# Kernel tuning notes

Measured on AMD Instinct MI355X. Metric: run time of the kernel, lower is better.

The kernel has to match this reference:

```python
import jax, jax.numpy as jnp
import numpy as np

B, S, H, Q = 32, 128, 128, 3  # users, seq_len, hidden_size, quadkey_level
L = Q - 1  # number of mixing scales


def setup_inputs() -> dict:
    key = jax.random.key(0)
    ks = jax.random.split(key, 12)
    trend0 = jax.random.normal(ks[0], (B, S, H), dtype=jnp.float32)
    trend1 = jax.random.normal(ks[1], (B, S, H), dtype=jnp.float32)
    trend2 = jax.random.normal(ks[2], (B, S, H), dtype=jnp.float32)
    # Per-position prefix linears padded into dense tensors, zero-masked beyond
    # the prefix length j+1 so the ragged math is exact:
    #   W1[j, :j+1, :j+1] ~ Linear(j+1, j+1), b1[j, :j+1]
    #   W2[j, :j+1]      ~ Linear(j+1, 1),   b2[j]
    idx = jnp.arange(S)
    pm = (idx[None, :] <= idx[:, None]).astype(jnp.float32)  # [j, s]: s <= j
    W1 = jax.random.normal(ks[3], (L, S, S, S), dtype=jnp.float32) * 0.05
    W1 = W1 * pm[None, :, :, None] * pm[None, :, None, :]
    b1 = jax.random.normal(ks[4], (L, S, S), dtype=jnp.float32) * 0.05 * pm[None]
    W2 = jax.random.normal(ks[5], (L, S, S), dtype=jnp.float32) * 0.05 * pm[None]
    b2 = jax.random.normal(ks[6], (L, S), dtype=jnp.float32) * 0.05
    # shared output MLP: Linear(H,H)->GELU->Linear(H,H); stored as [in, out]
    Wm1 = jax.random.normal(ks[7], (H, H), dtype=jnp.float32) * 0.05
    bm1 = jax.random.normal(ks[8], (H,), dtype=jnp.float32) * 0.05
    Wm2 = jax.random.normal(ks[9], (H, H), dtype=jnp.float32) * 0.05
    bm2 = jax.random.normal(ks[10], (H,), dtype=jnp.float32) * 0.05
    return {"trend0": trend0, "trend1": trend1, "trend2": trend2,
            "W1": W1, "b1": b1, "W2": W2, "b2": b2,
            "Wm1": Wm1, "bm1": bm1, "Wm2": Wm2, "bm2": bm2}


def reference(trend0, trend1, trend2, W1, b1, W2, b2, Wm1, bm1, Wm2, bm2):
    gelu = lambda x: jax.nn.gelu(x, approximate=False)  # torch nn.GELU default
    mlp = lambda x: gelu(x @ Wm1 + bm1) @ Wm2 + bm2

    rev = [trend2, trend1, trend0]  # trend_list reversed
    out_low = rev[0]
    out_high = rev[1]
    outs = [out_low]
    for i in range(Q - 1):
        # vectorized ragged prefix mix: per position j, out_low[:, :j+1] (as [B,H,j+1])
        # -> Linear(j+1,j+1) -> GELU -> Linear(j+1,1). Zero-padding in W1/b1/W2
        # kills all contributions beyond the prefix (GELU(0)=0).
        y1 = jnp.einsum('bsh,jst->bhjt', out_low, W1[i]) + b1[i]  # [B,H,S,S]
        res = jnp.einsum('bhjt,jt->bjh', gelu(y1), W2[i]) + b2[i][None, :, None]
        out_high = out_high + res
        out_low = out_high
        if i + 2 <= Q - 1:
            out_high = rev[i + 2]
        out_low = mlp(out_low)
        outs.append(out_low)
    outs.reverse()
    return tuple(outs)
```

## Files before the change

### kernel.cpp

```cpp
#include <hip/hip_runtime.h>
#include <stdint.h>

#define BSH (32 * 128 * 128)

typedef __attribute__((ext_vector_type(8))) __bf16 bf16x8;
typedef __attribute__((ext_vector_type(4))) float f32x4;

__device__ __forceinline__ unsigned short f2bf(float f) {
  union { float f; unsigned u; } v; v.f = f;
  return (unsigned short)((v.u + 0x7FFFu + ((v.u >> 16) & 1u)) >> 16);
}

__device__ __forceinline__ float fast_exp2(float x) {
#if __has_builtin(__builtin_amdgcn_exp2f)
  return __builtin_amdgcn_exp2f(x);
#else
  float r; asm("v_exp_f32 %0, %1" : "=v"(r) : "v"(x)); return r;
#endif
}
__device__ __forceinline__ float fast_rcp(float x) {
#if __has_builtin(__builtin_amdgcn_rcpf)
  return __builtin_amdgcn_rcpf(x);
#else
  float r; asm("v_rcp_f32 %0, %1" : "=v"(r) : "v"(x)); return r;
#endif
}

__device__ __forceinline__ float gelu_f(float y) {
  float u = y * y;
  float p = __builtin_fmaf(u, 0.044715f, 1.0f) * y;
  float w = fast_exp2(p * 2.30220787f);
  return y - y * fast_rcp(1.0f + w);
}

__device__ __forceinline__ void transpose_block_c(const float* __restrict__ src,
                                                  unsigned short* __restrict__ dst,
                                                  unsigned short* lds) {
  const int tid = threadIdx.x;
  const float4* s4 = (const float4*)src;
#pragma unroll
  for (int it = 0; it < 16; ++it) {
    int i4 = tid + it * 256;
    float4 v = s4[i4];
    int s = i4 >> 5;
    int t0 = (i4 * 4) & 127;
    int sc = s >> 3, se = s & 7;
#pragma unroll
    for (int e = 0; e < 4; ++e) {
      int t = t0 + e;
      lds[t * 136 + ((sc ^ ((t >> 2) & 7)) << 3) + se] = f2bf(((const float*)&v)[e]);
    }
  }
  __syncthreads();
#pragma unroll
  for (int it = 0; it < 8; ++it) {
    int c = tid + it * 256;
    int tr = c >> 4, sc = c & 15;
    uint4 d = *(const uint4*)(lds + tr * 136 + ((sc ^ ((tr >> 2) & 7)) << 3));
    *(uint4*)(dst + (sc * 128 + tr) * 8) = d;
  }
}

__global__ __launch_bounds__(256) void prepass_kernel(
    const float* __restrict__ W1, const float* __restrict__ trend2,
    const float* __restrict__ Wm1, const float* __restrict__ Wm2,
    unsigned short* __restrict__ W1Tc, unsigned short* __restrict__ T2c,
    unsigned short* __restrict__ Wm1c, unsigned short* __restrict__ Wm2c,
    float* __restrict__ out2) {
  __shared__ unsigned short lds[128 * 136];
  const int bid = blockIdx.x;
  if (bid < 256) {
    int x = bid & 7, i = bid >> 3;
    int stage = i >> 4, u = i & 15;
    int m = u & 7, half = u >> 3;
    int jpp = x + 8 * m;
    int j = half ? 127 - jpp : jpp;
    int blk = stage * 128 + j;
    transpose_block_c(W1 + blk * 16384, W1Tc + blk * 16384, lds);
  } else if (bid < 288) {
    const int b = bid - 256;
    transpose_block_c(trend2 + b * 16384, T2c + b * 16384, lds);
    const float4* s4 = (const float4*)(trend2 + b * 16384);
    float4* d4 = (float4*)(out2 + b * 16384);
#pragma unroll
    for (int it = 0; it < 16; ++it)
      d4[threadIdx.x + it * 256] = s4[threadIdx.x + it * 256];
  } else if (bid == 288) {
    transpose_block_c(Wm1, Wm1c, lds);
  } else {
    transpose_block_c(Wm2, Wm2c, lds);
  }
}

__global__ __launch_bounds__(128, 3) void mix_kernel(
    const unsigned short* __restrict__ XTc,
    const unsigned short* __restrict__ W1Tj,
    const float* __restrict__ b1j,
    const float* __restrict__ W2j,
    const float* __restrict__ b2j,
    const float* __restrict__ trendR,
    unsigned short* __restrict__ xoutc) {
  const int bid = blockIdx.x;
  const int b = bid >> 6;
  const int jp = bid & 63;
  const int js = jp, jb = 127 - jp;
  const int tid = threadIdx.x;
  const int p = tid >> 6;
  const int lane = tid & 63;
  const int lane15 = lane & 15;
  const int quad = lane >> 4;

  const int nt_s = (js >> 4) + 1, ks_s = (js >> 5) + 1;
  const int nt_b = (jb >> 4) + 1, ks_b = (jb >> 5) + 1;

  const unsigned short* Bp = XTc + b * 16384 + (p * 64 + lane15) * 8;
  const unsigned short* As = W1Tj + js * 16384 + lane15 * 8;
  const unsigned short* Ab = W1Tj + jb * 16384 + lane15 * 8;
  const float C = -2.45546937f;

  bf16x8 Bv[4][4];
#pragma unroll
  for (int ks = 0; ks < 4; ++ks)
    if (ks < ks_b) {
      const int ko = (ks * 4 + quad) * 1024;
      Bv[ks][0] = *(const bf16x8*)(Bp + ko);
      Bv[ks][1] = *(const bf16x8*)(Bp + ko + 128);
      Bv[ks][2] = *(const bf16x8*)(Bp + ko + 256);
      Bv[ks][3] = *(const bf16x8*)(Bp + ko + 384);
    }

  float psum[2][4];
#pragma unroll
  for (int jj = 0; jj < 2; ++jj)
#pragma unroll
    for (int ni = 0; ni < 4; ++ni) psum[jj][ni] = 0.f;

  for (int mt = 0; mt < nt_b; ++mt) {
    f32x4 acc[4];
#pragma unroll
    for (int ni = 0; ni < 4; ++ni) { f32x4 z = {0.f, 0.f, 0.f, 0.f}; acc[ni] = z; }
    const int mo = mt * 128;
#pragma unroll
    for (int ks = 0; ks < 4; ++ks)
      if (ks < ks_b) {
        bf16x8 a = *(const bf16x8*)(Ab + (ks * 4 + quad) * 1024 + mo);
        acc[0] = __builtin_amdgcn_mfma_f32_16x16x32_bf16(a, Bv[ks][0], acc[0], 0, 0, 0);
        acc[1] = __builtin_amdgcn_mfma_f32_16x16x32_bf16(a, Bv[ks][1], acc[1], 0, 0, 0);
        acc[2] = __builtin_amdgcn_mfma_f32_16x16x32_bf16(a, Bv[ks][2], acc[2], 0, 0, 0);
        acc[3] = __builtin_amdgcn_mfma_f32_16x16x32_bf16(a, Bv[ks][3], acc[3], 0, 0, 0);
      }
    const int tb = mt * 16 + quad * 4;
    float4 b1v = *(const float4*)(b1j + jb * 128 + tb);
    float4 w2v = *(const float4*)(W2j + jb * 128 + tb);
#pragma unroll
    for (int r = 0; r < 4; ++r) {
      float b1r = ((const float*)&b1v)[r];
      float w2r = ((const float*)&w2v)[r];
      float cb = C * b1r;
      float bw = b1r * w2r;
#pragma unroll
      for (int ni = 0; ni < 4; ++ni) {
        float a = acc[ni][r];
        float m = __builtin_fmaf(a, C, cb);
        float e = fast_exp2(m);
        float rr2 = fast_rcp(1.0f + e);
        float yw = __builtin_fmaf(a, w2r, bw);
        psum[1][ni] = __builtin_fmaf(yw, rr2, psum[1][ni]);
      }
    }
  }

  for (int mt = 0; mt < nt_s; ++mt) {
    f32x4 acc[4];
#pragma unroll
    for (int ni = 0; ni < 4; ++ni) { f32x4 z = {0.f, 0.f, 0.f, 0.f}; acc[ni] = z; }
    const int mo = mt * 128;
#pragma unroll
    for (int ks = 0; ks < 2; ++ks)
      if (ks < ks_s) {
        bf16x8 a = *(const bf16x8*)(As + (ks * 4 + quad) * 1024 + mo);
        acc[0] = __builtin_amdgcn_mfma_f32_16x16x32_bf16(a, Bv[ks][0], acc[0], 0, 0, 0);
        acc[1] = __builtin_amdgcn_mfma_f32_16x16x32_bf16(a, Bv[ks][1], acc[1], 0, 0, 0);
        acc[2] = __builtin_amdgcn_mfma_f32_16x16x32_bf16(a, Bv[ks][2], acc[2], 0, 0, 0);
        acc[3] = __builtin_amdgcn_mfma_f32_16x16x32_bf16(a, Bv[ks][3], acc[3], 0, 0, 0);
      }
    const int tb = mt * 16 + quad * 4;
    float4 b1v = *(const float4*)(b1j + js * 128 + tb);
    float4 w2v = *(const float4*)(W2j + js * 128 + tb);
#pragma unroll
    for (int r = 0; r < 4; ++r) {
      float b1r = ((const float*)&b1v)[r];
      float w2r = ((const float*)&w2v)[r];
      float cb = C * b1r;
      float bw = b1r * w2r;
#pragma unroll
      for (int ni = 0; ni < 4; ++ni) {
        float a = acc[ni][r];
        float m = __builtin_fmaf(a, C, cb);
        float e = fast_exp2(m);
        float rr2 = fast_rcp(1.0f + e);
        float yw = __builtin_fmaf(a, w2r, bw);
        psum[0][ni] = __builtin_fmaf(yw, rr2, psum[0][ni]);
      }
    }
  }

#pragma unroll
  for (int jj = 0; jj < 2; ++jj)
#pragma unroll
    for (int ni = 0; ni < 4; ++ni) {
      float v = psum[jj][ni];
      v += __shfl_xor(v, 16, 64);
      v += __shfl_xor(v, 32, 64);
      psum[jj][ni] = v;
    }

  if (quad == 0) {
#pragma unroll
    for (int jj = 0; jj < 2; ++jj) {
      const int j = jj ? jb : js;
      const float bias = b2j[j];
#pragma unroll
      for (int ni = 0; ni < 4; ++ni) {
        const int h = p * 64 + ni * 16 + lane15;
        float v = psum[jj][ni] + bias + trendR[(b * 128 + j) * 128 + h];
        xoutc[b * 16384 + ((h >> 3) * 128 + j) * 8 + (h & 7)] = f2bf(v);
      }
    }
  }
}

__global__ __launch_bounds__(256) void mlp_kernel(
    const unsigned short* __restrict__ Xc,
    const unsigned short* __restrict__ Wm1c,
    const unsigned short* __restrict__ Wm2c,
    const float* __restrict__ bm1,
    const float* __restrict__ bm2,
    float* __restrict__ outf,
    unsigned short* __restrict__ outTc,
    const int write_t) {
  __shared__ __align__(16) unsigned short U[16 * 128];
  __shared__ unsigned short ldsT[16 * 136];
  const int bid = blockIdx.x;
  const int b = bid >> 3;
  const int mb = bid & 7;
  const int tid = threadIdx.x;
  const int wave = tid >> 6;
  const int lane = tid & 63;
  const int lane15 = lane & 15;
  const int quad = lane >> 4;

  const unsigned short* Xb = Xc + b * 16384;

  f32x4 acc[2];
  { f32x4 z = {0.f, 0.f, 0.f, 0.f}; acc[0] = z; acc[1] = z; }
#pragma unroll
  for (int ks = 0; ks < 4; ++ks) {
    int kq = ks * 4 + quad;
    bf16x8 a  = *(const bf16x8*)(Xb + (kq * 128 + mb * 16 + lane15) * 8);
    bf16x8 w0 = *(const bf16x8*)(Wm1c + (kq * 128 + wave * 32 + lane15) * 8);
    bf16x8 w1 = *(const bf16x8*)(Wm1c + (kq * 128 + wave * 32 + 16 + lane15) * 8);
    acc[0] = __builtin_amdgcn_mfma_f32_16x16x32_bf16(a, w0, acc[0], 0, 0, 0);
    acc[1] = __builtin_amdgcn_mfma_f32_16x16x32_bf16(a, w1, acc[1], 0, 0, 0);
  }
#pragma unroll
  for (int ni = 0; ni < 2; ++ni) {
    int n = wave * 32 + ni * 16 + lane15;
    float bv = bm1[n];
#pragma unroll
    for (int r = 0; r < 4; ++r) {
      int jr = quad * 4 + r;
      U[((n >> 3) * 16 + jr) * 8 + (n & 7)] = f2bf(gelu_f(acc[ni][r] + bv));
    }
  }
  __syncthreads();
  { f32x4 z = {0.f, 0.f, 0.f, 0.f}; acc[0] = z; acc[1] = z; }
#pragma unroll
  for (int ks = 0; ks < 4; ++ks) {
    int kq = ks * 4 + quad;
    bf16x8 a  = *(const bf16x8*)(U + (kq * 16 + lane15) * 8);
    bf16x8 w0 = *(const bf16x8*)(Wm2c + (kq * 128 + wave * 32 + lane15) * 8);
    bf16x8 w1 = *(const bf16x8*)(Wm2c + (kq * 128 + wave * 32 + 16 + lane15) * 8);
    acc[0] = __builtin_amdgcn_mfma_f32_16x16x32_bf16(a, w0, acc[0], 0, 0, 0);
    acc[1] = __builtin_amdgcn_mfma_f32_16x16x32_bf16(a, w1, acc[1], 0, 0, 0);
  }
  {
    float* outb = outf + b * 16384 + mb * 16 * 128;
#pragma unroll
    for (int ni = 0; ni < 2; ++ni) {
      int n = wave * 32 + ni * 16 + lane15;
      float bv = bm2[n];
#pragma unroll
      for (int r = 0; r < 4; ++r) {
        int jr = quad * 4 + r;
        float v = acc[ni][r] + bv;
        outb[jr * 128 + n] = v;
        if (write_t) ldsT[jr * 136 + n] = f2bf(v);
      }
    }
  }
  if (write_t) {
    __syncthreads();
    int h = tid & 127, jr8 = tid >> 7;
    unsigned short tmp[8] __attribute__((aligned(16)));
#pragma unroll
    for (int e = 0; e < 8; ++e) tmp[e] = ldsT[(jr8 * 8 + e) * 136 + h];
    *(uint4*)(outTc + b * 16384 + ((mb * 2 + jr8) * 128 + h) * 8) = *(const uint4*)tmp;
  }
}

extern "C" void kernel_launch(void* const* d_in, const int* in_sizes, int n_in,
                              void* d_out, int out_size, void* d_ws, size_t ws_size,
                              hipStream_t stream) {
  (void)in_sizes; (void)n_in; (void)out_size; (void)ws_size;
  const float* trend0 = (const float*)d_in[0];
  const float* trend1 = (const float*)d_in[1];
  const float* trend2 = (const float*)d_in[2];
  const float* W1  = (const float*)d_in[3];
  const float* b1  = (const float*)d_in[4];
  const float* W2  = (const float*)d_in[5];
  const float* b2  = (const float*)d_in[6];
  const float* Wm1 = (const float*)d_in[7];
  const float* bm1 = (const float*)d_in[8];
  const float* Wm2 = (const float*)d_in[9];
  const float* bm2 = (const float*)d_in[10];
  float* out = (float*)d_out;
  char* ws = (char*)d_ws;

  unsigned short* W1Tc = (unsigned short*)(ws);
  unsigned short* T2c  = (unsigned short*)(ws + 8388608);
  unsigned short* x1c  = (unsigned short*)(ws + 9437184);
  unsigned short* A1Tc = (unsigned short*)(ws + 10485760);
  unsigned short* x2c  = (unsigned short*)(ws + 11534336);
  unsigned short* Wm1c = (unsigned short*)(ws + 12582912);
  unsigned short* Wm2c = (unsigned short*)(ws + 12615680);

  prepass_kernel<<<290, 256, 0, stream>>>(W1, trend2, Wm1, Wm2,
                                          W1Tc, T2c, Wm1c, Wm2c, out + 2 * BSH);
  mix_kernel<<<2048, 128, 0, stream>>>(T2c, W1Tc, b1, W2, b2, trend1, x1c);
  mlp_kernel<<<256, 256, 0, stream>>>(x1c, Wm1c, Wm2c, bm1, bm2,
                                      out + BSH, A1Tc, 1);
  mix_kernel<<<2048, 128, 0, stream>>>(A1Tc, W1Tc + 128 * 16384, b1 + 16384,
                                       W2 + 16384, b2 + 128, trend0, x2c);
  mlp_kernel<<<256, 256, 0, stream>>>(x2c, Wm1c, Wm2c, bm1, bm2,
                                      out, (unsigned short*)nullptr, 0);
}
```

Baseline: 138.5 us.

## Stage W1 tiles in LDS for mix kernel and simplify transpose

The mix kernel now copies the needed rows of the two W1 blocks (big and small prefix) into shared memory once, then feeds the MFMA A operands from LDS instead of re-reading global memory per M-tile. The transpose helper drops its XOR swizzle in favour of a plain padded layout with scalar gathers on read-out. The launch-bounds occupancy hint of 3 blocks is removed. The extra ~33KB of LDS per block and the new barrier may reduce occupancy, and the unswizzled scalar LDS reads in the transpose may cause bank conflicts.

```diff
diff --git a/kernel.cpp b/kernel.cpp
--- a/kernel.cpp
+++ b/kernel.cpp
@@ -37,27 +37,25 @@
                                                   unsigned short* __restrict__ dst,
                                                   unsigned short* lds) {
   const int tid = threadIdx.x;
-  const float4* s4 = (const float4*)src;
+  const float4* s4 = (const float4*)(src);
 #pragma unroll
   for (int it = 0; it < 16; ++it) {
     int i4 = tid + it * 256;
     float4 v = s4[i4];
     int s = i4 >> 5;
     int t0 = (i4 * 4) & 127;
-    int sc = s >> 3, se = s & 7;
-#pragma unroll
-    for (int e = 0; e < 4; ++e) {
-      int t = t0 + e;
-      lds[t * 136 + ((sc ^ ((t >> 2) & 7)) << 3) + se] = f2bf(((const float*)&v)[e]);
-    }
+    unsigned short* pp = lds + s * 136 + t0;
+    pp[0] = f2bf(v.x); pp[1] = f2bf(v.y); pp[2] = f2bf(v.z); pp[3] = f2bf(v.w);
   }
   __syncthreads();
 #pragma unroll
   for (int it = 0; it < 8; ++it) {
     int c = tid + it * 256;
-    int tr = c >> 4, sc = c & 15;
-    uint4 d = *(const uint4*)(lds + tr * 136 + ((sc ^ ((tr >> 2) & 7)) << 3));
-    *(uint4*)(dst + (sc * 128 + tr) * 8) = d;
+    int sc = c >> 7, tr = c & 127;
+    unsigned short tmp[8] __attribute__((aligned(16)));
+#pragma unroll
+    for (int e = 0; e < 8; ++e) tmp[e] = lds[(sc * 8 + e) * 136 + tr];
+    *(uint4*)(dst + (sc * 128 + tr) * 8) = *(const uint4*)tmp;
   }
 }
 
@@ -92,7 +90,7 @@
   }
 }
 
-__global__ __launch_bounds__(128, 3) void mix_kernel(
+__global__ __launch_bounds__(128) void mix_kernel(
     const unsigned short* __restrict__ XTc,
     const unsigned short* __restrict__ W1Tj,
     const float* __restrict__ b1j,
@@ -100,6 +98,7 @@
     const float* __restrict__ b2j,
     const float* __restrict__ trendR,
     unsigned short* __restrict__ xoutc) {
+  __shared__ __align__(16) unsigned short Alds[16896];
   const int bid = blockIdx.x;
   const int b = bid >> 6;
   const int jp = bid & 63;
@@ -112,10 +111,10 @@
 
   const int nt_s = (js >> 4) + 1, ks_s = (js >> 5) + 1;
   const int nt_b = (jb >> 4) + 1, ks_b = (jb >> 5) + 1;
+  const int m16b = nt_b * 16, m16s = nt_s * 16;
+  const int base_s = ks_b * nt_b * 512;
 
   const unsigned short* Bp = XTc + b * 16384 + (p * 64 + lane15) * 8;
-  const unsigned short* As = W1Tj + js * 16384 + lane15 * 8;
-  const unsigned short* Ab = W1Tj + jb * 16384 + lane15 * 8;
   const float C = -2.45546937f;
 
   bf16x8 Bv[4][4];
@@ -129,6 +128,20 @@
       Bv[ks][3] = *(const bf16x8*)(Bp + ko + 384);
     }
 
+  {
+    const unsigned short* Ab = W1Tj + jb * 16384;
+    for (int kq = 0; kq < 4 * ks_b; ++kq)
+      if (tid < m16b)
+        *(uint4*)(Alds + (kq * m16b + tid) * 8) =
+            *(const uint4*)(Ab + (kq * 128 + tid) * 8);
+    const unsigned short* As = W1Tj + js * 16384;
+    for (int kq = 0; kq < 4 * ks_s; ++kq)
+      if (tid < m16s)
+        *(uint4*)(Alds + base_s + (kq * m16s + tid) * 8) =
+            *(const uint4*)(As + (kq * 128 + tid) * 8);
+  }
+  __syncthreads();
+
   float psum[2][4];
 #pragma unroll
   for (int jj = 0; jj < 2; ++jj)
@@ -139,11 +152,11 @@
     f32x4 acc[4];
 #pragma unroll
     for (int ni = 0; ni < 4; ++ni) { f32x4 z = {0.f, 0.f, 0.f, 0.f}; acc[ni] = z; }
-    const int mo = mt * 128;
+    const int mo = mt * 16 + lane15;
 #pragma unroll
     for (int ks = 0; ks < 4; ++ks)
       if (ks < ks_b) {
-        bf16x8 a = *(const bf16x8*)(Ab + (ks * 4 + quad) * 1024 + mo);
+        bf16x8 a = *(const bf16x8*)(Alds + ((ks * 4 + quad) * m16b + mo) * 8);
         acc[0] = __builtin_amdgcn_mfma_f32_16x16x32_bf16(a, Bv[ks][0], acc[0], 0, 0, 0);
         acc[1] = __builtin_amdgcn_mfma_f32_16x16x32_bf16(a, Bv[ks][1], acc[1], 0, 0, 0);
         acc[2] = __builtin_amdgcn_mfma_f32_16x16x32_bf16(a, Bv[ks][2], acc[2], 0, 0, 0);
@@ -174,11 +187,11 @@
     f32x4 acc[4];
 #pragma unroll
     for (int ni = 0; ni < 4; ++ni) { f32x4 z = {0.f, 0.f, 0.f, 0.f}; acc[ni] = z; }
-    const int mo = mt * 128;
+    const int mo = mt * 16 + lane15;
 #pragma unroll
     for (int ks = 0; ks < 2; ++ks)
       if (ks < ks_s) {
-        bf16x8 a = *(const bf16x8*)(As + (ks * 4 + quad) * 1024 + mo);
+        bf16x8 a = *(const bf16x8*)(Alds + base_s + ((ks * 4 + quad) * m16s + mo) * 8);
         acc[0] = __builtin_amdgcn_mfma_f32_16x16x32_bf16(a, Bv[ks][0], acc[0], 0, 0, 0);
         acc[1] = __builtin_amdgcn_mfma_f32_16x16x32_bf16(a, Bv[ks][1], acc[1], 0, 0, 0);
         acc[2] = __builtin_amdgcn_mfma_f32_16x16x32_bf16(a, Bv[ks][2], acc[2], 0, 0, 0);
```

New measurement: 145.5 us. 1.05x slower.

## Split mix kernel M-tiles across four waves and simplify prepass transpose

Applied to the files above, without the earlier changes.

The mix kernel now launches 256 threads per block. Two wave pairs each take alternating M-tiles and their partial sums are reduced through shared memory before the bf16 output is written. This doubles the waves working on each (batch, j-pair) block to hide latency, at the cost of duplicated B-fragment loads and an extra barrier. The prepass transpose also drops the XOR swizzle in favour of row-major LDS writes followed by strided 8-element gathers, which may add LDS bank conflicts.

```diff
diff --git a/kernel.cpp b/kernel.cpp
--- a/kernel.cpp
+++ b/kernel.cpp
@@ -37,27 +37,25 @@
                                                   unsigned short* __restrict__ dst,
                                                   unsigned short* lds) {
   const int tid = threadIdx.x;
-  const float4* s4 = (const float4*)src;
+  const float4* s4 = (const float4*)(src);
 #pragma unroll
   for (int it = 0; it < 16; ++it) {
     int i4 = tid + it * 256;
     float4 v = s4[i4];
     int s = i4 >> 5;
     int t0 = (i4 * 4) & 127;
-    int sc = s >> 3, se = s & 7;
-#pragma unroll
-    for (int e = 0; e < 4; ++e) {
-      int t = t0 + e;
-      lds[t * 136 + ((sc ^ ((t >> 2) & 7)) << 3) + se] = f2bf(((const float*)&v)[e]);
-    }
+    unsigned short* pp = lds + s * 136 + t0;
+    pp[0] = f2bf(v.x); pp[1] = f2bf(v.y); pp[2] = f2bf(v.z); pp[3] = f2bf(v.w);
   }
   __syncthreads();
 #pragma unroll
   for (int it = 0; it < 8; ++it) {
     int c = tid + it * 256;
-    int tr = c >> 4, sc = c & 15;
-    uint4 d = *(const uint4*)(lds + tr * 136 + ((sc ^ ((tr >> 2) & 7)) << 3));
-    *(uint4*)(dst + (sc * 128 + tr) * 8) = d;
+    int sc = c >> 7, tr = c & 127;
+    unsigned short tmp[8] __attribute__((aligned(16)));
+#pragma unroll
+    for (int e = 0; e < 8; ++e) tmp[e] = lds[(sc * 8 + e) * 136 + tr];
+    *(uint4*)(dst + (sc * 128 + tr) * 8) = *(const uint4*)tmp;
   }
 }
 
@@ -92,7 +90,7 @@
   }
 }
 
-__global__ __launch_bounds__(128, 3) void mix_kernel(
+__global__ __launch_bounds__(256, 3) void mix_kernel(
     const unsigned short* __restrict__ XTc,
     const unsigned short* __restrict__ W1Tj,
     const float* __restrict__ b1j,
@@ -100,12 +98,15 @@
     const float* __restrict__ b2j,
     const float* __restrict__ trendR,
     unsigned short* __restrict__ xoutc) {
+  __shared__ float res[512];
   const int bid = blockIdx.x;
   const int b = bid >> 6;
   const int jp = bid & 63;
   const int js = jp, jb = 127 - jp;
   const int tid = threadIdx.x;
-  const int p = tid >> 6;
+  const int wave = tid >> 6;
+  const int p = wave & 1;
+  const int mh = wave >> 1;
   const int lane = tid & 63;
   const int lane15 = lane & 15;
   const int quad = lane >> 4;
@@ -135,7 +136,7 @@
 #pragma unroll
     for (int ni = 0; ni < 4; ++ni) psum[jj][ni] = 0.f;
 
-  for (int mt = 0; mt < nt_b; ++mt) {
+  for (int mt = mh; mt < nt_b; mt += 2) {
     f32x4 acc[4];
 #pragma unroll
     for (int ni = 0; ni < 4; ++ni) { f32x4 z = {0.f, 0.f, 0.f, 0.f}; acc[ni] = z; }
@@ -170,7 +171,7 @@
     }
   }
 
-  for (int mt = 0; mt < nt_s; ++mt) {
+  for (int mt = mh; mt < nt_s; mt += 2) {
     f32x4 acc[4];
 #pragma unroll
     for (int ni = 0; ni < 4; ++ni) { f32x4 z = {0.f, 0.f, 0.f, 0.f}; acc[ni] = z; }
@@ -217,16 +218,22 @@
 
   if (quad == 0) {
 #pragma unroll
-    for (int jj = 0; jj < 2; ++jj) {
-      const int j = jj ? jb : js;
-      const float bias = b2j[j];
-#pragma unroll
-      for (int ni = 0; ni < 4; ++ni) {
-        const int h = p * 64 + ni * 16 + lane15;
-        float v = psum[jj][ni] + bias + trendR[(b * 128 + j) * 128 + h];
-        xoutc[b * 16384 + ((h >> 3) * 128 + j) * 8 + (h & 7)] = f2bf(v);
-      }
-    }
+    for (int jj = 0; jj < 2; ++jj)
+#pragma unroll
+      for (int ni = 0; ni < 4; ++ni)
+        res[wave * 128 + jj * 64 + ni * 16 + lane15] = psum[jj][ni];
+  }
+  __syncthreads();
+  {
+    const int l = tid & 15;
+    const int ni = (tid >> 4) & 3;
+    const int jj = (tid >> 6) & 1;
+    const int pp = tid >> 7;
+    const int j = jj ? jb : js;
+    const int h = pp * 64 + ni * 16 + l;
+    float v = res[tid] + res[tid + 256] + b2j[j] +
+              trendR[(b * 128 + j) * 128 + h];
+    xoutc[b * 16384 + ((h >> 3) * 128 + j) * 8 + (h & 7)] = f2bf(v);
   }
 }
 
@@ -337,10 +344,10 @@
 
   prepass_kernel<<<290, 256, 0, stream>>>(W1, trend2, Wm1, Wm2,
                                           W1Tc, T2c, Wm1c, Wm2c, out + 2 * BSH);
-  mix_kernel<<<2048, 128, 0, stream>>>(T2c, W1Tc, b1, W2, b2, trend1, x1c);
+  mix_kernel<<<2048, 256, 0, stream>>>(T2c, W1Tc, b1, W2, b2, trend1, x1c);
   mlp_kernel<<<256, 256, 0, stream>>>(x1c, Wm1c, Wm2c, bm1, bm2,
                                       out + BSH, A1Tc, 1);
-  mix_kernel<<<2048, 128, 0, stream>>>(A1Tc, W1Tc + 128 * 16384, b1 + 16384,
+  mix_kernel<<<2048, 256, 0, stream>>>(A1Tc, W1Tc + 128 * 16384, b1 + 16384,
                                        W2 + 16384, b2 + 128, trend0, x2c);
   mlp_kernel<<<256, 256, 0, stream>>>(x2c, Wm1c, Wm2c, bm1, bm2,
                                       out, (unsigned short*)nullptr, 0);
```

New measurement: 138.1 us (median of 2 runs). Within noise of the previous version (-0.3%).
